# Kernel tuning notes

Measured on AMD Instinct MI355X. Metric: run time of the kernel, lower is better.

Reference implementation:

```python
import jax, jax.numpy as jnp
import numpy as np

# BoeNet deterministic (greedy) BFS rollout reference.
# Assumptions (source truncated): GrowthPolicyNet ~ Linear(H,1)+sigmoid applied to
# node hidden + DEPTH_EMBED_SCALE * depth_embedding; greedy path expands when
# prob > greedy_threshold. Tree is materialized as a complete binary tree up to
# max_depth with per-node active masks (jit-friendly; honors data-dependent growth
# via masking instead of dynamic shapes). Pooling: mean over active nodes.

V, E, H = 32000, 512, 512
MAX_DEPTH = 3
DEPTH_EMBED_SCALE = 0.01
GREEDY_THRESHOLD = 0.5
PROB_MIN, PROB_MAX = 1e-7, 1.0 - 1e-7
EPS = 1e-8
SIB_SCALE = 1.0 / np.sqrt(H)


def setup_inputs() -> dict:
    key = jax.random.key(0)
    ks = jax.random.split(key, 8)
    B, S = 8, 512
    return {
        "tokens": jax.random.randint(ks[0], (B, S), 0, V),
        "emb": jax.random.normal(ks[1], (V, E), jnp.float32) * 0.02,
        "Wp": jax.random.normal(ks[2], (E, H), jnp.float32) / np.sqrt(E),
        "bp": jnp.zeros((H,), jnp.float32),
        "Wc": jax.random.normal(ks[3], (H, 2 * H), jnp.float32) / np.sqrt(H),
        "bc": jnp.zeros((2 * H,), jnp.float32),
        "Wg": jax.random.normal(ks[4], (H, 1), jnp.float32) / np.sqrt(H),
        "bg": jnp.zeros((1,), jnp.float32),
        "dep": jax.random.normal(ks[5], (MAX_DEPTH + 1, H), jnp.float32) * 0.01,
        "sib": jax.random.normal(ks[6], (2, H), jnp.float32) * 0.02,
        "Wout": jax.random.normal(ks[7], (H, V), jnp.float32) / np.sqrt(H),
        "bout": jnp.zeros((V,), jnp.float32),
    }


def reference(tokens, emb, Wp, bp, Wc, bc, Wg, bg, dep, sib, Wout, bout):
    B, S = tokens.shape
    N = B * S
    # h0: embedding lookup + projection, flattened to positions [N, H]
    h0 = (emb[tokens.reshape(N)] @ Wp + bp)  # [N, H]

    nodes = h0[:, None, :]                    # [N, 1, H] level-0 nodes
    active = jnp.ones((N, 1), h0.dtype)
    agg_sum = h0                              # root always counted
    agg_count = jnp.ones((N,), h0.dtype)

    for d in range(MAX_DEPTH):
        n = nodes.shape[1]
        # growth policy: sigmoid gate on node hidden + scaled depth embedding
        gate_in = nodes + DEPTH_EMBED_SCALE * dep[d]
        prob = jax.nn.sigmoid(jnp.einsum('nkh,ho->nko', gate_in, Wg)[..., 0] + bg[0])
        prob = jnp.clip(prob, PROB_MIN, PROB_MAX)           # [N, n]
        expand = (prob > GREEDY_THRESHOLD).astype(h0.dtype) * active  # [N, n]
        # children: Linear(H, 2H) split into left/right, plus sibling embeddings
        ch = (jnp.einsum('nkh,hj->nkj', nodes, Wc) + bc).reshape(N, 2 * n, H)
        sib_idx = jnp.tile(jnp.arange(2), n)                # [0,1,0,1,...]
        ch = ch + SIB_SCALE * sib[sib_idx]
        ch_active = jnp.repeat(expand, 2, axis=1)           # [N, 2n]
        agg_sum = agg_sum + jnp.einsum('nkh,nk->nh', ch, ch_active)
        agg_count = agg_count + ch_active.sum(axis=1)
        nodes, active = ch, ch_active

    pooled = agg_sum / jnp.maximum(agg_count, EPS)[:, None]  # mean pooling
    logits = pooled @ Wout + bout                            # [N, V]
    return logits.reshape(B, S, V)
```

## Files before the change

### kernel.cpp

```cpp
#include <hip/hip_runtime.h>
#include <cstdint>

#define BM 128
#define BN 128
#define BK 32

typedef __attribute__((ext_vector_type(8))) short short8;
typedef _Float16 half8 __attribute__((ext_vector_type(8)));
typedef __attribute__((ext_vector_type(4))) float floatx4;

union H8 { short8 s; half8 h; };

static constexpr float SIBS   = 0.044194173824159216f;
static constexpr float LS_INV = 1.0f / 2048.0f;

__device__ __forceinline__ unsigned short f2bf(float x){
    union { float f; unsigned u32; } v; v.f = x;
    unsigned r = ((v.u32 >> 16) & 1u) + 0x7fffu;
    return (unsigned short)((v.u32 + r) >> 16);
}
__device__ __forceinline__ void split_f16(float x, unsigned short& h, unsigned short& s){
    _Float16 hh = (_Float16)x;
    _Float16 ss = (_Float16)((x - (float)hh) * 2048.0f);
    union { _Float16 f; unsigned short u; } a, b;
    a.f = hh; b.f = ss;
    h = a.u; s = b.u;
}

#define GLDS(g, l) __builtin_amdgcn_global_load_lds( \
    (const __attribute__((address_space(1))) void*)(g), \
    (__attribute__((address_space(3))) void*)(l), 16, 0, 0)

__global__ void prep_all(const float* __restrict__ Wp, const float* __restrict__ Wc,
                         const float* __restrict__ Wout, const float* __restrict__ Wg,
                         const float* __restrict__ bg, const float* __restrict__ dep,
                         unsigned short* __restrict__ WpT_h, unsigned short* __restrict__ WpT_l,
                         unsigned short* __restrict__ WcT_h, unsigned short* __restrict__ WcT_l,
                         unsigned short* __restrict__ Wc2T_h, unsigned short* __restrict__ Wc2T_l,
                         unsigned short* __restrict__ WoutT,
                         float* __restrict__ gacc, float* __restrict__ cgate)
{
    int bid = blockIdx.x;
    if (bid >= 17024){
        if (bid < 17032){
            int base = (bid - 17024)*3584 + threadIdx.x;
#pragma unroll
            for (int k = 0; k < 14; k++) gacc[base + k*256] = 0.f;
        } else {
            int wv = threadIdx.x >> 6, l = threadIdx.x & 63;
            if (wv < 3){
                float s = 0.f;
#pragma unroll
                for (int t = 0; t < 8; t++){
                    int h = t*64 + l;
                    s += dep[wv*512 + h] * Wg[h];
                }
#pragma unroll
                for (int off = 32; off > 0; off >>= 1) s += __shfl_down(s, off);
                if (l == 0) cgate[wv] = 0.01f*s + bg[0];
            }
        }
        return;
    }
    __shared__ float t[32][33];
    const float* src = nullptr;
    unsigned short *dh = nullptr, *dl = nullptr;
    int C = 512, bx, by; bool sum2 = false;
    if (bid < 256){ src=Wp; dh=WpT_h; dl=WpT_l; C=512; bx=bid&15; by=bid>>4; }
    else if (bid < 768){ int rel=bid-256; src=Wc; dh=WcT_h; dl=WcT_l; C=1024; bx=rel&31; by=rel>>5; }
    else if (bid < 1024){ int rel=bid-768; src=Wc; dh=Wc2T_h; dl=Wc2T_l; C=512; sum2=true; bx=rel&15; by=rel>>4; }
    else { int rel=bid-1024; src=Wout; dh=WoutT; dl=nullptr; C=32000; bx=rel%1000; by=rel/1000; }
    int c0 = bx*32, r0 = by*32;
    int tx = threadIdx.x & 31, ty = threadIdx.x >> 5;
#pragma unroll
    for (int k = 0; k < 4; k++){
        int r = ty + k*8;
        float x;
        if (sum2) x = Wc[(size_t)(r0+r)*1024 + c0+tx] + Wc[(size_t)(r0+r)*1024 + 512 + c0+tx];
        else      x = src[(size_t)(r0+r)*C + c0+tx];
        t[r][tx] = x;
    }
    __syncthreads();
#pragma unroll
    for (int k = 0; k < 4; k++){
        int r = ty + k*8;
        float x = t[tx][r];
        size_t o = (size_t)(c0+r)*512 + r0+tx;
        if (dl){
            unsigned short h, s; split_f16(x, h, s);
            dh[o] = h; dl[o] = s;
        } else {
            dh[o] = f2bf(x);
        }
    }
}

template<int MODE, int DEPTH>
__global__ __launch_bounds__(256, 2)
void gemm_k(const unsigned short* __restrict__ Abf,
            const unsigned short* __restrict__ Agh,
            const unsigned short* __restrict__ Agl,
            const unsigned short* __restrict__ BTh,
            const unsigned short* __restrict__ BTl,
            const float* __restrict__ bias,
            const int* __restrict__ tokens,
            const float* __restrict__ emb,
            const float* __restrict__ sib,
            const float* __restrict__ Wg,
            float* __restrict__ gacc,
            const float* __restrict__ mArr,
            const float* __restrict__ cinv,
            const float* __restrict__ h0,
            float* __restrict__ nodes_next,
            unsigned short* __restrict__ nxh,
            unsigned short* __restrict__ nxl,
            float* __restrict__ f32out,
            unsigned short* __restrict__ pooled,
            float* __restrict__ out,
            int N)
{
    constexpr int K = 512;
    __shared__ __align__(16) unsigned short Ah[BM*BK];
    __shared__ __align__(16) unsigned short Al[BM*BK];
    __shared__ __align__(16) unsigned short Bh[BK*BN];
    __shared__ __align__(16) unsigned short Bl[BK*BN];

    const int tid = threadIdx.x;
    const int w = tid >> 6, l = tid & 63;
    const int wr = w >> 1, wc = w & 1;

    int bx, by;
    if (MODE == 2){
        int bid = blockIdx.x;
        int swz = (bid & 7) * 1000 + (bid >> 3);
        bx = swz & 31; by = swz >> 5;
    } else {
        bx = blockIdx.x; by = blockIdx.y;
    }
    const int row0 = bx * BM;
    const int n0   = by * BN;
    const int q = l >> 4, lm = l & 15;

    floatx4 acc[4][4]  = {};
    floatx4 accx[4][4] = {};

    const float* aptr = nullptr;
    const int am = tid & 127, kq0 = tid >> 7;
    if (MODE == 0) aptr = emb + (long)tokens[row0 + am] * K;

    long arow0 = 0, arow1 = 0;
    if (MODE != 0){
        arow0 = (long)(row0 + l) * K;
        arow1 = (long)(row0 + 64 + l) * K;
    }
    const long brow0 = (long)(n0 + l) * K;
    const long brow1 = (long)(n0 + 64 + l) * K;

    for (int k0 = 0; k0 < K; k0 += BK){
        __syncthreads();
        GLDS(BTh + brow0 + k0 + w*8, (char*)Bh + w*2048);
        GLDS(BTh + brow1 + k0 + w*8, (char*)Bh + w*2048 + 1024);
        if (MODE != 2){
            GLDS(BTl + brow0 + k0 + w*8, (char*)Bl + w*2048);
            GLDS(BTl + brow1 + k0 + w*8, (char*)Bl + w*2048 + 1024);
        }
        if (MODE == 1 || MODE == 3){
            GLDS(Agh + arow0 + k0 + w*8, (char*)Ah + w*2048);
            GLDS(Agh + arow1 + k0 + w*8, (char*)Ah + w*2048 + 1024);
            GLDS(Agl + arow0 + k0 + w*8, (char*)Al + w*2048);
            GLDS(Agl + arow1 + k0 + w*8, (char*)Al + w*2048 + 1024);
        } else if (MODE == 2){
            GLDS(Abf + arow0 + k0 + w*8, (char*)Ah + w*2048);
            GLDS(Abf + arow1 + k0 + w*8, (char*)Ah + w*2048 + 1024);
        } else {
#pragma unroll
            for (int t = 0; t < 2; t++){
                int kq = kq0 + 2*t;
                const float* src = aptr + k0 + kq*8;
                float xs[8];
                *(floatx4*)&xs[0] = *(const floatx4*)(src);
                *(floatx4*)&xs[4] = *(const floatx4*)(src + 4);
                unsigned short h8[8], l8[8];
#pragma unroll
                for (int e = 0; e < 8; e++) split_f16(xs[e], h8[e], l8[e]);
                int s = kq*128 + am;
                *(short8*)&Ah[s*8] = *(const short8*)h8;
                *(short8*)&Al[s*8] = *(const short8*)l8;
            }
        }
        __syncthreads();

        H8 bh[4], bl[4];
#pragma unroll
        for (int j = 0; j < 4; j++){
            bh[j].s = *(const short8*)&Bh[(q*128 + wc*64 + j*16 + lm)*8];
            if (MODE != 2)
                bl[j].s = *(const short8*)&Bl[(q*128 + wc*64 + j*16 + lm)*8];
        }
#pragma unroll
        for (int i = 0; i < 4; i++){
            H8 ah; ah.s = *(const short8*)&Ah[(q*128 + wr*64 + i*16 + lm)*8];
            if (MODE != 2){
                H8 al; al.s = *(const short8*)&Al[(q*128 + wr*64 + i*16 + lm)*8];
#pragma unroll
                for (int j = 0; j < 4; j++)
                    acc[i][j]  = __builtin_amdgcn_mfma_f32_16x16x32_f16(ah.h, bh[j].h, acc[i][j], 0, 0, 0);
#pragma unroll
                for (int j = 0; j < 4; j++)
                    accx[i][j] = __builtin_amdgcn_mfma_f32_16x16x32_f16(ah.h, bl[j].h, accx[i][j], 0, 0, 0);
#pragma unroll
                for (int j = 0; j < 4; j++)
                    accx[i][j] = __builtin_amdgcn_mfma_f32_16x16x32_f16(al.h, bh[j].h, accx[i][j], 0, 0, 0);
            } else {
#pragma unroll
                for (int j = 0; j < 4; j++)
                    acc[i][j] = __builtin_amdgcn_mfma_f32_16x16x32_bf16(ah.s, bh[j].s, acc[i][j], 0, 0, 0);
            }
        }
    }

    float wgj[4];
    if (MODE <= 1){
#pragma unroll
        for (int j = 0; j < 4; j++)
            wgj[j] = Wg[(n0 + wc*64 + j*16 + lm) & 511];
    }
    const int halfc = n0 >> 9;

#pragma unroll
    for (int i = 0; i < 4; i++){
        int rbase = row0 + wr*64 + i*16 + q*4;
        float gp[4] = {0.f, 0.f, 0.f, 0.f};
#pragma unroll
        for (int j = 0; j < 4; j++){
            int col = n0 + wc*64 + j*16 + lm;
            float badd = 0.f, bsum = 0.f;
            if (MODE == 0 || MODE == 2) badd = bias[col];
            if (MODE == 1) badd = bias[col] + SIBS * sib[halfc*512 + (col & 511)];
            if (MODE == 3)
                bsum = bias[col] + bias[512 + col] + SIBS * (sib[col] + sib[512 + col]);
#pragma unroll
            for (int r = 0; r < 4; r++){
                int row = rbase + r;
                float v = acc[i][j][r];
                if (MODE != 2) v += accx[i][j][r] * LS_INV;
                if (MODE == 0){
                    v += badd;
                    gp[r] += v * wgj[j];
                    long o = (long)row*512 + col;
                    f32out[o] = v;
                    unsigned short hh, ss; split_f16(v, hh, ss);
                    nxh[o] = hh; nxl[o] = ss;
                } else if (MODE == 1){
                    v += badd;
                    gp[r] += v * wgj[j];
                    long o = (long)(2*row + halfc)*512 + (col & 511);
                    nodes_next[o] = v;
                    if (DEPTH == 0){
                        unsigned short hh, ss; split_f16(v, hh, ss);
                        nxh[o] = hh; nxl[o] = ss;
                    }
                } else if (MODE == 3){
                    long o = (long)row*512 + col;
                    float outv = (h0[o] + v + mArr[row]*bsum) * cinv[row];
                    pooled[o] = f2bf(outv);
                } else {
                    out[(long)row*(long)N + col] = v + badd;
                }
            }
        }
        if (MODE <= 1){
#pragma unroll
            for (int r = 0; r < 4; r++){
                float s = gp[r];
                s += __shfl_xor(s, 1);
                s += __shfl_xor(s, 2);
                s += __shfl_xor(s, 4);
                s += __shfl_xor(s, 8);
                if (lm == 0){
                    int row = rbase + r;
                    int grow = (MODE == 0) ? row : (2*row + halfc);
                    atomicAdd(&gacc[grow], s);
                }
            }
        }
    }
}

__global__ void msum_k(const float* __restrict__ nodes0,
                       const float* __restrict__ nodes1,
                       const float* __restrict__ nodes2,
                       const float* __restrict__ gacc,
                       const float* __restrict__ cgate,
                       unsigned short* __restrict__ Sh,
                       unsigned short* __restrict__ Sl,
                       float* __restrict__ mArr,
                       float* __restrict__ cinv)
{
    int n = blockIdx.x;
    const float* g0 = gacc;
    const float* g1 = gacc + 4096;
    const float* g2 = gacc + 12288;
    float c0 = cgate[0], c1 = cgate[1], c2 = cgate[2];
    bool b0  =  g0[n]       + c0 > 0.f;
    bool b10 = (g1[2*n]     + c1 > 0.f) && b0;
    bool b11 = (g1[2*n + 1] + c1 > 0.f) && b0;
    bool b20 = (g2[4*n]     + c2 > 0.f) && b10;
    bool b21 = (g2[4*n + 1] + c2 > 0.f) && b10;
    bool b22 = (g2[4*n + 2] + c2 > 0.f) && b11;
    bool b23 = (g2[4*n + 3] + c2 > 0.f) && b11;
    float a0  = (float)b0;
    float a10 = (float)b10, a11 = (float)b11;
    float a20 = (float)b20, a21 = (float)b21, a22 = (float)b22, a23 = (float)b23;
    if (threadIdx.x == 0){
        float m = a0 + a10 + a11 + a20 + a21 + a22 + a23;
        mArr[n] = m;
        cinv[n] = 1.f / (1.f + 2.f * m);
    }
    const float* p0 = nodes0 + (long)n * 512;
    const float* p1 = nodes1 + (long)(2*n) * 512;
    const float* p2 = nodes2 + (long)(4*n) * 512;
    for (int c = threadIdx.x; c < 512; c += 256){
        float s = a0 * p0[c]
                + a10 * p1[c]        + a11 * p1[512 + c]
                + a20 * p2[c]        + a21 * p2[512 + c]
                + a22 * p2[1024 + c] + a23 * p2[1536 + c];
        unsigned short hh, ss; split_f16(s, hh, ss);
        long o = (long)n * 512 + c;
        Sh[o] = hh; Sl[o] = ss;
    }
}

extern "C" void kernel_launch(void* const* d_in, const int* in_sizes, int n_in,
                              void* d_out, int out_size, void* d_ws, size_t ws_size,
                              hipStream_t stream)
{
    const int*   tokens = (const int*)d_in[0];
    const float* emb    = (const float*)d_in[1];
    const float* Wp     = (const float*)d_in[2];
    const float* bp     = (const float*)d_in[3];
    const float* Wc     = (const float*)d_in[4];
    const float* bc     = (const float*)d_in[5];
    const float* Wg     = (const float*)d_in[6];
    const float* bg     = (const float*)d_in[7];
    const float* dep    = (const float*)d_in[8];
    const float* sib    = (const float*)d_in[9];
    const float* Wout   = (const float*)d_in[10];
    const float* bout   = (const float*)d_in[11];

    if (ws_size < ((size_t)48 << 20)) return;

    char* w = (char*)d_ws;
    auto alloc = [&](size_t bytes)->char*{
        char* p = w; w += (bytes + 255) & ~(size_t)255; return p;
    };
    unsigned short* WpT_h  = (unsigned short*)alloc((size_t)512*512*2);
    unsigned short* WpT_l  = (unsigned short*)alloc((size_t)512*512*2);
    unsigned short* WcT_h  = (unsigned short*)alloc((size_t)1024*512*2);
    unsigned short* WcT_l  = (unsigned short*)alloc((size_t)1024*512*2);
    unsigned short* Wc2T_h = (unsigned short*)alloc((size_t)512*512*2);
    unsigned short* Wc2T_l = (unsigned short*)alloc((size_t)512*512*2);
    unsigned short* WoutT  = (unsigned short*)alloc((size_t)32000*512*2);
    unsigned short* pooled = (unsigned short*)alloc((size_t)4096*512*2);
    float*          gacc   = (float*)alloc((size_t)28672*4);
    float*          cgate  = (float*)alloc(256);

    char* ob = (char*)d_out;
    float*          nodes0 = (float*)(ob + ((size_t) 64 << 20));
    unsigned short* n0h    = (unsigned short*)(ob + ((size_t) 80 << 20));
    unsigned short* n0l    = (unsigned short*)(ob + ((size_t) 88 << 20));
    float*          nodes1 = (float*)(ob + ((size_t) 96 << 20));
    unsigned short* n1h    = (unsigned short*)(ob + ((size_t)128 << 20));
    unsigned short* n1l    = (unsigned short*)(ob + ((size_t)144 << 20));
    float*          nodes2 = (float*)(ob + ((size_t)160 << 20));
    unsigned short* Sh     = (unsigned short*)(ob + ((size_t)200 << 20));
    unsigned short* Sl     = (unsigned short*)(ob + ((size_t)208 << 20));
    float*          mArr   = (float*)(ob + ((size_t)216 << 20));
    float*          cinvA  = (float*)(ob + ((size_t)217 << 20));
    float*          out    = (float*)d_out;

    prep_all<<<17033, 256, 0, stream>>>(Wp, Wc, Wout, Wg, bg, dep,
        WpT_h, WpT_l, WcT_h, WcT_l, Wc2T_h, Wc2T_l, WoutT, gacc, cgate);

    gemm_k<0,0><<<dim3(32, 4), 256, 0, stream>>>(nullptr, nullptr, nullptr,
        WpT_h, WpT_l, bp, tokens, emb, nullptr, Wg, gacc,
        nullptr, nullptr, nullptr, nullptr, n0h, n0l, nodes0, nullptr, nullptr, 512);

    gemm_k<1,0><<<dim3(32, 8), 256, 0, stream>>>(nullptr, n0h, n0l,
        WcT_h, WcT_l, bc, nullptr, nullptr, sib, Wg, gacc + 4096,
        nullptr, nullptr, nullptr, nodes1, n1h, n1l, nullptr, nullptr, nullptr, 1024);

    gemm_k<1,1><<<dim3(64, 8), 256, 0, stream>>>(nullptr, n1h, n1l,
        WcT_h, WcT_l, bc, nullptr, nullptr, sib, Wg, gacc + 12288,
        nullptr, nullptr, nullptr, nodes2, nullptr, nullptr, nullptr, nullptr, nullptr, 1024);

    msum_k<<<4096, 256, 0, stream>>>(nodes0, nodes1, nodes2, gacc, cgate,
        Sh, Sl, mArr, cinvA);

    gemm_k<3,0><<<dim3(32, 4), 256, 0, stream>>>(nullptr, Sh, Sl,
        Wc2T_h, Wc2T_l, bc, nullptr, nullptr, sib, nullptr, nullptr,
        mArr, cinvA, nodes0, nullptr, nullptr, nullptr, nullptr, pooled, nullptr, 512);

    gemm_k<2,0><<<dim3(8000), 256, 0, stream>>>(pooled, nullptr, nullptr,
        WoutT, nullptr, bout, nullptr, nullptr, nullptr, nullptr, nullptr,
        nullptr, nullptr, nullptr, nullptr, nullptr, nullptr, nullptr, nullptr, out, 32000);
}
```

Measured before the change: 1.003 ms.

## Add dedicated pipelined bf16 output GEMM with larger tiles and swizzled LDS

Moves the final vocab projection GEMM (the dominant cost, 4096x32000x512) out of the generic gemm_k into a dedicated kernel. The new kernel uses 256x128 tiles with 512 threads and BK=64. It keeps a triple-buffered LDS pipeline with explicit vmcnt waits, XOR-swizzled LDS addressing to avoid bank conflicts, and s_setprio around the MFMA block. The aim is to hide global load latency and raise MFMA utilisation, at the cost of more LDS per block (about 144KB) and therefore lower occupancy.

Measured after the change: 959.1 us. 1.05x faster.

```diff
diff --git a/kernel.cpp b/kernel.cpp
--- a/kernel.cpp
+++ b/kernel.cpp
@@ -97,8 +97,7 @@
 
 template<int MODE, int DEPTH>
 __global__ __launch_bounds__(256, 2)
-void gemm_k(const unsigned short* __restrict__ Abf,
-            const unsigned short* __restrict__ Agh,
+void gemm_k(const unsigned short* __restrict__ Agh,
             const unsigned short* __restrict__ Agl,
             const unsigned short* __restrict__ BTh,
             const unsigned short* __restrict__ BTl,
@@ -116,7 +115,6 @@
             unsigned short* __restrict__ nxl,
             float* __restrict__ f32out,
             unsigned short* __restrict__ pooled,
-            float* __restrict__ out,
             int N)
 {
     constexpr int K = 512;
@@ -128,17 +126,8 @@
     const int tid = threadIdx.x;
     const int w = tid >> 6, l = tid & 63;
     const int wr = w >> 1, wc = w & 1;
-
-    int bx, by;
-    if (MODE == 2){
-        int bid = blockIdx.x;
-        int swz = (bid & 7) * 1000 + (bid >> 3);
-        bx = swz & 31; by = swz >> 5;
-    } else {
-        bx = blockIdx.x; by = blockIdx.y;
-    }
-    const int row0 = bx * BM;
-    const int n0   = by * BN;
+    const int row0 = blockIdx.x * BM;
+    const int n0   = blockIdx.y * BN;
     const int q = l >> 4, lm = l & 15;
 
     floatx4 acc[4][4]  = {};
@@ -160,18 +149,13 @@
         __syncthreads();
         GLDS(BTh + brow0 + k0 + w*8, (char*)Bh + w*2048);
         GLDS(BTh + brow1 + k0 + w*8, (char*)Bh + w*2048 + 1024);
-        if (MODE != 2){
-            GLDS(BTl + brow0 + k0 + w*8, (char*)Bl + w*2048);
-            GLDS(BTl + brow1 + k0 + w*8, (char*)Bl + w*2048 + 1024);
-        }
+        GLDS(BTl + brow0 + k0 + w*8, (char*)Bl + w*2048);
+        GLDS(BTl + brow1 + k0 + w*8, (char*)Bl + w*2048 + 1024);
         if (MODE == 1 || MODE == 3){
             GLDS(Agh + arow0 + k0 + w*8, (char*)Ah + w*2048);
             GLDS(Agh + arow1 + k0 + w*8, (char*)Ah + w*2048 + 1024);
             GLDS(Agl + arow0 + k0 + w*8, (char*)Al + w*2048);
             GLDS(Agl + arow1 + k0 + w*8, (char*)Al + w*2048 + 1024);
-        } else if (MODE == 2){
-            GLDS(Abf + arow0 + k0 + w*8, (char*)Ah + w*2048);
-            GLDS(Abf + arow1 + k0 + w*8, (char*)Ah + w*2048 + 1024);
         } else {
 #pragma unroll
             for (int t = 0; t < 2; t++){
@@ -194,28 +178,21 @@
 #pragma unroll
         for (int j = 0; j < 4; j++){
             bh[j].s = *(const short8*)&Bh[(q*128 + wc*64 + j*16 + lm)*8];
-            if (MODE != 2)
-                bl[j].s = *(const short8*)&Bl[(q*128 + wc*64 + j*16 + lm)*8];
+            bl[j].s = *(const short8*)&Bl[(q*128 + wc*64 + j*16 + lm)*8];
         }
 #pragma unroll
         for (int i = 0; i < 4; i++){
             H8 ah; ah.s = *(const short8*)&Ah[(q*128 + wr*64 + i*16 + lm)*8];
-            if (MODE != 2){
-                H8 al; al.s = *(const short8*)&Al[(q*128 + wr*64 + i*16 + lm)*8];
-#pragma unroll
-                for (int j = 0; j < 4; j++)
-                    acc[i][j]  = __builtin_amdgcn_mfma_f32_16x16x32_f16(ah.h, bh[j].h, acc[i][j], 0, 0, 0);
-#pragma unroll
-                for (int j = 0; j < 4; j++)
-                    accx[i][j] = __builtin_amdgcn_mfma_f32_16x16x32_f16(ah.h, bl[j].h, accx[i][j], 0, 0, 0);
-#pragma unroll
-                for (int j = 0; j < 4; j++)
-                    accx[i][j] = __builtin_amdgcn_mfma_f32_16x16x32_f16(al.h, bh[j].h, accx[i][j], 0, 0, 0);
-            } else {
-#pragma unroll
-                for (int j = 0; j < 4; j++)
-                    acc[i][j] = __builtin_amdgcn_mfma_f32_16x16x32_bf16(ah.s, bh[j].s, acc[i][j], 0, 0, 0);
-            }
+            H8 al; al.s = *(const short8*)&Al[(q*128 + wr*64 + i*16 + lm)*8];
+#pragma unroll
+            for (int j = 0; j < 4; j++)
+                acc[i][j]  = __builtin_amdgcn_mfma_f32_16x16x32_f16(ah.h, bh[j].h, acc[i][j], 0, 0, 0);
+#pragma unroll
+            for (int j = 0; j < 4; j++)
+                accx[i][j] = __builtin_amdgcn_mfma_f32_16x16x32_f16(ah.h, bl[j].h, accx[i][j], 0, 0, 0);
+#pragma unroll
+            for (int j = 0; j < 4; j++)
+                accx[i][j] = __builtin_amdgcn_mfma_f32_16x16x32_f16(al.h, bh[j].h, accx[i][j], 0, 0, 0);
         }
     }
 
@@ -235,15 +212,14 @@
         for (int j = 0; j < 4; j++){
             int col = n0 + wc*64 + j*16 + lm;
             float badd = 0.f, bsum = 0.f;
-            if (MODE == 0 || MODE == 2) badd = bias[col];
+            if (MODE == 0) badd = bias[col];
             if (MODE == 1) badd = bias[col] + SIBS * sib[halfc*512 + (col & 511)];
             if (MODE == 3)
                 bsum = bias[col] + bias[512 + col] + SIBS * (sib[col] + sib[512 + col]);
 #pragma unroll
             for (int r = 0; r < 4; r++){
                 int row = rbase + r;
-                float v = acc[i][j][r];
-                if (MODE != 2) v += accx[i][j][r] * LS_INV;
+                float v = acc[i][j][r] + accx[i][j][r] * LS_INV;
                 if (MODE == 0){
                     v += badd;
                     gp[r] += v * wgj[j];
@@ -260,12 +236,10 @@
                         unsigned short hh, ss; split_f16(v, hh, ss);
                         nxh[o] = hh; nxl[o] = ss;
                     }
-                } else if (MODE == 3){
+                } else {
                     long o = (long)row*512 + col;
                     float outv = (h0[o] + v + mArr[row]*bsum) * cinv[row];
                     pooled[o] = f2bf(outv);
-                } else {
-                    out[(long)row*(long)N + col] = v + badd;
                 }
             }
         }
@@ -283,6 +257,106 @@
                     atomicAdd(&gacc[grow], s);
                 }
             }
+        }
+    }
+}
+
+__global__ __launch_bounds__(512, 2)
+void gemm_out(const unsigned short* __restrict__ pooled,
+              const unsigned short* __restrict__ BT,
+              const float* __restrict__ bout,
+              float* __restrict__ out)
+{
+    constexpr int K = 512;
+    constexpr int NT = 8;
+    constexpr int BUFS = 24576;
+    __shared__ __align__(16) unsigned short lds[3 * BUFS];
+
+    const int tid = threadIdx.x;
+    const int w = tid >> 6, l = tid & 63;
+    const int wm = w >> 1, wn = w & 1;
+    const int q = l >> 4, lm = l & 15;
+
+    const int bid = blockIdx.x;
+    const int swz = (bid & 7) * 500 + (bid >> 3);
+    const int m0 = (swz & 15) * 256;
+    const int n0 = (swz >> 4) * 128;
+
+    const int lr = l >> 3;
+    const int kq = (l & 7) ^ (lr & 7);
+    long asrc[4]; long bsrc[2];
+#pragma unroll
+    for (int a = 0; a < 4; a++){
+        int t = w + 8*a;
+        asrc[a] = (long)(m0 + t*8 + lr) * K + kq*8;
+    }
+#pragma unroll
+    for (int b = 0; b < 2; b++){
+        int t = w + 8*b;
+        bsrc[b] = (long)(n0 + t*8 + lr) * K + kq*8;
+    }
+
+    auto ostage = [&](int u){
+        unsigned short* base = lds + (u % 3) * BUFS;
+        const int k0 = u * 64;
+#pragma unroll
+        for (int a = 0; a < 4; a++)
+            GLDS(pooled + asrc[a] + k0, (char*)base + (w + 8*a)*1024);
+#pragma unroll
+        for (int b = 0; b < 2; b++)
+            GLDS(BT + bsrc[b] + k0, (char*)base + 32768 + (w + 8*b)*1024);
+    };
+
+    floatx4 acc[4][4] = {};
+
+    ostage(0); ostage(1);
+
+#pragma unroll
+    for (int u = 0; u < NT; u++){
+        if (u < NT-2) ostage(u+2);
+        if (u < NT-2)       asm volatile("s_waitcnt vmcnt(12)" ::: "memory");
+        else if (u == NT-2) asm volatile("s_waitcnt vmcnt(6)"  ::: "memory");
+        else                asm volatile("s_waitcnt vmcnt(0)"  ::: "memory");
+        __builtin_amdgcn_s_barrier();
+        __builtin_amdgcn_sched_barrier(0);
+
+        const unsigned short* base  = lds + (u % 3) * BUFS;
+        const unsigned short* bbase = base + 16384;
+#pragma unroll
+        for (int s = 0; s < 2; s++){
+            H8 aF[4], bF[4];
+#pragma unroll
+            for (int i = 0; i < 4; i++){
+                int row = wm*64 + i*16 + lm;
+                aF[i].s = *(const short8*)&base[(row*8 + ((s*4+q) ^ (lm&7)))*8];
+            }
+#pragma unroll
+            for (int j = 0; j < 4; j++){
+                int col = wn*64 + j*16 + lm;
+                bF[j].s = *(const short8*)&bbase[(col*8 + ((s*4+q) ^ (lm&7)))*8];
+            }
+            __builtin_amdgcn_s_setprio(1);
+#pragma unroll
+            for (int i = 0; i < 4; i++)
+#pragma unroll
+                for (int j = 0; j < 4; j++)
+                    acc[i][j] = __builtin_amdgcn_mfma_f32_16x16x32_bf16(aF[i].s, bF[j].s, acc[i][j], 0, 0, 0);
+            __builtin_amdgcn_s_setprio(0);
+        }
+        __builtin_amdgcn_s_barrier();
+        __builtin_amdgcn_sched_barrier(0);
+    }
+
+#pragma unroll
+    for (int i = 0; i < 4; i++){
+        int rbase = m0 + wm*64 + i*16 + q*4;
+#pragma unroll
+        for (int j = 0; j < 4; j++){
+            int col = n0 + wn*64 + j*16 + lm;
+            float badd = bout[col];
+#pragma unroll
+            for (int r = 0; r < 4; r++)
+                out[(long)(rbase + r)*32000L + col] = acc[i][j][r] + badd;
         }
     }
 }
@@ -382,26 +456,24 @@
     prep_all<<<17033, 256, 0, stream>>>(Wp, Wc, Wout, Wg, bg, dep,
         WpT_h, WpT_l, WcT_h, WcT_l, Wc2T_h, Wc2T_l, WoutT, gacc, cgate);
 
-    gemm_k<0,0><<<dim3(32, 4), 256, 0, stream>>>(nullptr, nullptr, nullptr,
+    gemm_k<0,0><<<dim3(32, 4), 256, 0, stream>>>(nullptr, nullptr,
         WpT_h, WpT_l, bp, tokens, emb, nullptr, Wg, gacc,
-        nullptr, nullptr, nullptr, nullptr, n0h, n0l, nodes0, nullptr, nullptr, 512);
-
-    gemm_k<1,0><<<dim3(32, 8), 256, 0, stream>>>(nullptr, n0h, n0l,
+        nullptr, nullptr, nullptr, nullptr, n0h, n0l, nodes0, nullptr, 512);
+
+    gemm_k<1,0><<<dim3(32, 8), 256, 0, stream>>>(n0h, n0l,
         WcT_h, WcT_l, bc, nullptr, nullptr, sib, Wg, gacc + 4096,
-        nullptr, nullptr, nullptr, nodes1, n1h, n1l, nullptr, nullptr, nullptr, 1024);
-
-    gemm_k<1,1><<<dim3(64, 8), 256, 0, stream>>>(nullptr, n1h, n1l,
+        nullptr, nullptr, nullptr, nodes1, n1h, n1l, nullptr, nullptr, 1024);
+
+    gemm_k<1,1><<<dim3(64, 8), 256, 0, stream>>>(n1h, n1l,
         WcT_h, WcT_l, bc, nullptr, nullptr, sib, Wg, gacc + 12288,
-        nullptr, nullptr, nullptr, nodes2, nullptr, nullptr, nullptr, nullptr, nullptr, 1024);
+        nullptr, nullptr, nullptr, nodes2, nullptr, nullptr, nullptr, nullptr, 1024);
 
     msum_k<<<4096, 256, 0, stream>>>(nodes0, nodes1, nodes2, gacc, cgate,
         Sh, Sl, mArr, cinvA);
 
-    gemm_k<3,0><<<dim3(32, 4), 256, 0, stream>>>(nullptr, Sh, Sl,
+    gemm_k<3,0><<<dim3(32, 4), 256, 0, stream>>>(Sh, Sl,
         Wc2T_h, Wc2T_l, bc, nullptr, nullptr, sib, nullptr, nullptr,
-        mArr, cinvA, nodes0, nullptr, nullptr, nullptr, nullptr, pooled, nullptr, 512);
-
-    gemm_k<2,0><<<dim3(8000), 256, 0, stream>>>(pooled, nullptr, nullptr,
-        WoutT, nullptr, bout, nullptr, nullptr, nullptr, nullptr, nullptr,
-        nullptr, nullptr, nullptr, nullptr, nullptr, nullptr, nullptr, nullptr, out, 32000);
-}
+        mArr, cinvA, nodes0, nullptr, nullptr, nullptr, nullptr, pooled, 512);
+
+    gemm_out<<<4000, 512, 0, stream>>>(pooled, WoutT, bout, out);
+}
```
